# Optimization experiments

Measured on AMD Instinct MI355X. Metric: run time of the kernel, lower is better.

The kernel has to match this reference:

```python
import jax, jax.numpy as jnp
import numpy as np

B, N, F_IN, F_OUT = 4, 2048, 256, 128
ALPHA = 0.2  # LeakyReLU negative slope
EPS = 1e-5   # LayerNorm eps
NEG = -9e15


def setup_inputs() -> dict:
    key = jax.random.key(0)
    k1, k2, k3, k4 = jax.random.split(key, 4)
    h = jax.random.normal(k1, (B, N, F_IN), dtype=jnp.float32)
    adj = jax.random.randint(k2, (B, N, N), 0, 2, dtype=jnp.int32)
    # xavier_uniform with gain=1.414 for W
    limW = 1.414 * np.sqrt(6.0 / (F_IN + F_OUT))
    W = jax.random.uniform(k3, (F_IN, F_OUT), dtype=jnp.float32, minval=-limW, maxval=limW)
    # kaiming_uniform (leaky_relu, a=alpha, fan_in=2*F_OUT) for a
    gain = np.sqrt(2.0 / (1.0 + ALPHA ** 2))
    lima = gain * np.sqrt(3.0 / (2 * F_OUT))
    a = jax.random.uniform(k4, (2 * F_OUT, 1), dtype=jnp.float32, minval=-lima, maxval=lima)
    gamma = jnp.ones((F_OUT,), dtype=jnp.float32)
    beta = jnp.zeros((F_OUT,), dtype=jnp.float32)
    return {"h": h, "adj": adj, "W": W, "a": a, "gamma": gamma, "beta": beta}


def reference(h, adj, W, a, gamma, beta):
    Wh = jnp.einsum("bnf,fo->bno", h, W)            # [B,N,F_out]
    a1, a2 = a[:F_OUT, 0], a[F_OUT:, 0]              # [F_out] each
    s1 = Wh @ a1                                      # [B,N] score of node i
    s2 = Wh @ a2                                      # [B,N] score of node j
    # e[b,i,j] = LeakyReLU(s1[b,i] + s2[b,j])  -- avoids O(N^2*2F) concat tensor
    e = s1[:, :, None] + s2[:, None, :]
    e = jnp.where(e >= 0, e, ALPHA * e)
    e = jnp.where(adj > 0, e, NEG)
    attention = jax.nn.softmax(e, axis=2)             # [B,N,N]
    h_prime = jnp.einsum("bij,bjo->bio", attention, Wh)
    mu = jnp.mean(h_prime, axis=-1, keepdims=True)
    var = jnp.var(h_prime, axis=-1, keepdims=True)
    h_norm = (h_prime - mu) / jnp.sqrt(var + EPS) * gamma + beta
    return jax.nn.gelu(h_norm, approximate=False)
```

## Files before the change

kernel.cpp:

```cpp
#include <hip/hip_runtime.h>
#include <hip/hip_bf16.h>

typedef __attribute__((ext_vector_type(8))) short bf16x8;
typedef __attribute__((ext_vector_type(4))) float f32x4;

#define NB   4
#define NN   2048
#define FIN  256
#define FOUT 128
#define SPLIT 4
#define JCH  (NN / SPLIT)
#define NSTEP (JCH / 64)

__device__ __forceinline__ unsigned short f2bf(float f) {
    unsigned int u = __builtin_bit_cast(unsigned int, f);
    u += 0x7fffu + ((u >> 16) & 1u);
    return (unsigned short)(u >> 16);
}
__device__ __forceinline__ float bf2f(unsigned short s) {
    return __builtin_bit_cast(float, (unsigned int)s << 16);
}

__global__ __launch_bounds__(256) void k_wt(const float* __restrict__ W,
                                            unsigned short* __restrict__ WT) {
    int idx = blockIdx.x * 256 + threadIdx.x;
    int k = idx & 255, o = idx >> 8;
    WT[idx] = f2bf(W[k * FOUT + o]);
}

__global__ __launch_bounds__(256) void k_wh(const float* __restrict__ h,
                                            const float* __restrict__ a,
                                            const unsigned short* __restrict__ WT,
                                            unsigned short* __restrict__ WhB,
                                            float* __restrict__ s1,
                                            float* __restrict__ s2) {
    __shared__ unsigned short hs[16][264];
    __shared__ float s1w[4][16], s2w[4][16];
    int t = threadIdx.x, blk = blockIdx.x;
    int nglob0 = blk * 16;
    int b = nglob0 >> 11;

    const float4* h4 = (const float4*)h + (size_t)blk * 1024;
    #pragma unroll
    for (int i = 0; i < 4; ++i) {
        int idx = i * 256 + t;
        float4 v = h4[idx];
        int row = idx >> 6, c4 = (idx & 63) * 4;
        unsigned int lo = (unsigned int)f2bf(v.x) | ((unsigned int)f2bf(v.y) << 16);
        unsigned int hi = (unsigned int)f2bf(v.z) | ((unsigned int)f2bf(v.w) << 16);
        *(uint2*)&hs[row][c4] = make_uint2(lo, hi);
    }
    __syncthreads();

    int w = t >> 6, l = t & 63, lr = l & 15, lk = l >> 4;
    float a1v[2], a2v[2];
    #pragma unroll
    for (int j = 0; j < 2; ++j) {
        a1v[j] = a[(w * 2 + j) * 16 + lr];
        a2v[j] = a[FOUT + (w * 2 + j) * 16 + lr];
    }
    f32x4 acc[2] = {{0.f,0.f,0.f,0.f},{0.f,0.f,0.f,0.f}};

    #pragma unroll
    for (int kk = 0; kk < 8; ++kk) {
        int k0 = kk * 32;
        bf16x8 af = *(const bf16x8*)&hs[lr][k0 + lk * 8];
        #pragma unroll
        for (int j = 0; j < 2; ++j) {
            bf16x8 bfr = *(const bf16x8*)(WT + ((w * 2 + j) * 16 + lr) * 256 + k0 + lk * 8);
            acc[j] = __builtin_amdgcn_mfma_f32_16x16x32_bf16(af, bfr, acc[j], 0, 0, 0);
        }
    }

    int n0 = nglob0 & 2047;
    int sIdx = n0 >> 6;
    int hh   = (n0 >> 5) & 1;
    int bklo = (n0 & 31) >> 3;
    float v1[4] = {0.f,0.f,0.f,0.f}, v2[4] = {0.f,0.f,0.f,0.f};
    #pragma unroll
    for (int j = 0; j < 2; ++j) {
        int ot = w * 2 + j;
        float x0 = acc[j][0], x1 = acc[j][1], x2 = acc[j][2], x3 = acc[j][3];
        ushort4 pk;
        pk.x = f2bf(x0); pk.y = f2bf(x1); pk.z = f2bf(x2); pk.w = f2bf(x3);
        size_t fragBase = (((size_t)(b * 8 + ot) * 32 + sIdx) * 2 + hh) * 64;
        size_t lane = fragBase + lr + 16 * (bklo + (lk >> 1));
        *(ushort4*)(WhB + lane * 8 + (lk & 1) * 4) = pk;
        v1[0] += x0 * a1v[j]; v1[1] += x1 * a1v[j]; v1[2] += x2 * a1v[j]; v1[3] += x3 * a1v[j];
        v2[0] += x0 * a2v[j]; v2[1] += x1 * a2v[j]; v2[2] += x2 * a2v[j]; v2[3] += x3 * a2v[j];
    }
    #pragma unroll
    for (int m = 1; m < 16; m <<= 1)
        #pragma unroll
        for (int r = 0; r < 4; ++r) {
            v1[r] += __shfl_xor(v1[r], m);
            v2[r] += __shfl_xor(v2[r], m);
        }
    if (lr == 0)
        #pragma unroll
        for (int r = 0; r < 4; ++r) {
            s1w[w][lk * 4 + r] = v1[r];
            s2w[w][lk * 4 + r] = v2[r];
        }
    __syncthreads();
    if (t < 16) {
        s1[nglob0 + t] = s1w[0][t] + s1w[1][t] + s1w[2][t] + s1w[3][t];
        s2[nglob0 + t] = s2w[0][t] + s2w[1][t] + s2w[2][t] + s2w[3][t];
    }
}

__global__ __launch_bounds__(256) void k_attn(const int* __restrict__ adj,
                                              const unsigned short* __restrict__ WhB,
                                              const float* __restrict__ s1,
                                              const float* __restrict__ s2,
                                              unsigned short* __restrict__ num,
                                              float* __restrict__ Zp) {
    __shared__ union {
        unsigned short Ps[2][64][76];
        float hS[64][132];
    } S;
    __shared__ float s2S[JCH];

    int t = threadIdx.x, w = t >> 6, l = t & 63, lr = l & 15, lk = l >> 4;
    int bid = blockIdx.x;
    int bi = (bid >> 3) + (bid & 7) * 64;
    int part = bi >> 7, rem = bi & 127;
    int b = rem >> 5, i0 = (rem & 31) * 64, j0 = part * JCH;

    if (t < 128) ((float4*)s2S)[t] = ((const float4*)(s2 + b * NN + j0))[t];
    float s1r = s1[b * NN + i0 + w * 16 + lr];

    const int* aRow = adj + ((size_t)(b * NN) + i0 + w * 16 + lr) * NN + j0 + lk * 16;
    int4 av[2][4];
    #pragma unroll
    for (int s = 0; s < 2; ++s)
        #pragma unroll
        for (int q = 0; q < 4; ++q)
            av[s][q] = *(const int4*)(aRow + s * 64 + q * 4);

    const unsigned short* B0 = WhB + (((size_t)(b * 8 + w * 2) * 32 + part * NSTEP) * 2) * 512 + (size_t)l * 8;
    const unsigned short* B1 = B0 + (size_t)32 * 2 * 512;
    bf16x8 bB[2][2][2];
    #pragma unroll
    for (int s = 0; s < 2; ++s) {
        bB[s][0][0] = *(const bf16x8*)(B0 + s * 1024);
        bB[s][0][1] = *(const bf16x8*)(B0 + s * 1024 + 512);
        bB[s][1][0] = *(const bf16x8*)(B1 + s * 1024);
        bB[s][1][1] = *(const bf16x8*)(B1 + s * 1024 + 512);
    }

    f32x4 acc[4][2];
    #pragma unroll
    for (int rg = 0; rg < 4; ++rg) {
        acc[rg][0] = (f32x4){0.f,0.f,0.f,0.f};
        acc[rg][1] = (f32x4){0.f,0.f,0.f,0.f};
    }
    float zacc = 0.f;

    __syncthreads();

    #pragma unroll
    for (int s = 0; s < NSTEP; ++s) {
        const int slot = s & 1;
        int4 m0 = av[slot][0], m1 = av[slot][1], m2 = av[slot][2], m3 = av[slot][3];
        if (s < NSTEP - 2) {
            #pragma unroll
            for (int q = 0; q < 4; ++q)
                av[slot][q] = *(const int4*)(aRow + (s + 2) * 64 + q * 4);
        }

        {
            int mv[16] = {m0.x, m0.y, m0.z, m0.w, m1.x, m1.y, m1.z, m1.w,
                          m2.x, m2.y, m2.z, m2.w, m3.x, m3.y, m3.z, m3.w};
            const float* sp = &s2S[s * 64 + lk * 16];
            float4 f0 = *(const float4*)sp,       f1 = *(const float4*)(sp + 4);
            float4 f2 = *(const float4*)(sp + 8), f3 = *(const float4*)(sp + 12);
            float sv[16] = {f0.x,f0.y,f0.z,f0.w, f1.x,f1.y,f1.z,f1.w,
                            f2.x,f2.y,f2.z,f2.w, f3.x,f3.y,f3.z,f3.w};
            unsigned int pw[8];
            #pragma unroll
            for (int q = 0; q < 8; ++q) {
                float e0 = s1r + sv[2 * q];
                float e1 = s1r + sv[2 * q + 1];
                e0 = fmaxf(e0, 0.2f * e0);
                e1 = fmaxf(e1, 0.2f * e1);
                float p0 = (mv[2 * q]     > 0) ? __expf(e0) : 0.f;
                float p1 = (mv[2 * q + 1] > 0) ? __expf(e1) : 0.f;
                zacc += p0 + p1;
                pw[q] = (unsigned int)f2bf(p0) | ((unsigned int)f2bf(p1) << 16);
            }
            *(uint4*)&S.Ps[slot][w * 16 + lr][lk * 16]     = (uint4){pw[0], pw[1], pw[2], pw[3]};
            *(uint4*)&S.Ps[slot][w * 16 + lr][lk * 16 + 8] = (uint4){pw[4], pw[5], pw[6], pw[7]};
        }
        asm volatile("s_waitcnt lgkmcnt(0)" ::: "memory");
        __builtin_amdgcn_s_barrier();
        __builtin_amdgcn_sched_barrier(0);

        bf16x8 c00 = bB[slot][0][0], c01 = bB[slot][0][1];
        bf16x8 c10 = bB[slot][1][0], c11 = bB[slot][1][1];
        if (s < NSTEP - 2) {
            bB[slot][0][0] = *(const bf16x8*)(B0 + (s + 2) * 1024);
            bB[slot][0][1] = *(const bf16x8*)(B0 + (s + 2) * 1024 + 512);
            bB[slot][1][0] = *(const bf16x8*)(B1 + (s + 2) * 1024);
            bB[slot][1][1] = *(const bf16x8*)(B1 + (s + 2) * 1024 + 512);
        }

        #pragma unroll
        for (int rg = 0; rg < 4; ++rg) {
            bf16x8 a0 = *(const bf16x8*)&S.Ps[slot][rg * 16 + lr][lk * 8];
            bf16x8 a1 = *(const bf16x8*)&S.Ps[slot][rg * 16 + lr][32 + lk * 8];
            acc[rg][0] = __builtin_amdgcn_mfma_f32_16x16x32_bf16(a0, c00, acc[rg][0], 0, 0, 0);
            acc[rg][0] = __builtin_amdgcn_mfma_f32_16x16x32_bf16(a1, c01, acc[rg][0], 0, 0, 0);
            acc[rg][1] = __builtin_amdgcn_mfma_f32_16x16x32_bf16(a0, c10, acc[rg][1], 0, 0, 0);
            acc[rg][1] = __builtin_amdgcn_mfma_f32_16x16x32_bf16(a1, c11, acc[rg][1], 0, 0, 0);
        }
    }

    zacc += __shfl_xor(zacc, 16);
    zacc += __shfl_xor(zacc, 32);
    if (l < 16) Zp[(size_t)(part * NB + b) * NN + i0 + w * 16 + l] = zacc;

    __syncthreads();
    #pragma unroll
    for (int rg = 0; rg < 4; ++rg)
        #pragma unroll
        for (int ot2 = 0; ot2 < 2; ++ot2)
            #pragma unroll
            for (int r = 0; r < 4; ++r)
                S.hS[rg * 16 + lk * 4 + r][(w * 2 + ot2) * 16 + lr] = acc[rg][ot2][r];
    __syncthreads();

    unsigned short* np = num + ((size_t)(part * NB + b) * NN + i0) * FOUT;
    #pragma unroll
    for (int q = 0; q < 4; ++q) {
        int flat = q * 256 + t;
        int row = flat >> 4, c8 = (flat & 15) * 8;
        float4 v0 = *(const float4*)&S.hS[row][c8];
        float4 v1 = *(const float4*)&S.hS[row][c8 + 4];
        uint4 pk;
        pk.x = (unsigned int)f2bf(v0.x) | ((unsigned int)f2bf(v0.y) << 16);
        pk.y = (unsigned int)f2bf(v0.z) | ((unsigned int)f2bf(v0.w) << 16);
        pk.z = (unsigned int)f2bf(v1.x) | ((unsigned int)f2bf(v1.y) << 16);
        pk.w = (unsigned int)f2bf(v1.z) | ((unsigned int)f2bf(v1.w) << 16);
        *(uint4*)(np + (size_t)row * FOUT + c8) = pk;
    }
}

__global__ __launch_bounds__(256) void k_final(const unsigned short* __restrict__ num,
                                               const float* __restrict__ Zp,
                                               const float* __restrict__ gamma,
                                               const float* __restrict__ beta,
                                               float* __restrict__ out) {
    int t = threadIdx.x, bi = blockIdx.x;
    int rowA = t >> 5;
    int c0 = (t & 31) * 4;
    size_t gn = (size_t)bi * 8 + rowA;
    int b = (int)(gn >> 11), n = (int)(gn & 2047);

    float Z = 0.f;
    #pragma unroll
    for (int p = 0; p < SPLIT; ++p) Z += Zp[(size_t)(p * NB + b) * NN + n];

    float x[4] = {0.f, 0.f, 0.f, 0.f};
    #pragma unroll
    for (int p = 0; p < SPLIT; ++p) {
        const unsigned short* np = num + ((size_t)(p * NB + b) * NN + n) * FOUT + c0;
        ushort4 u = *(const ushort4*)np;
        x[0] += bf2f(u.x); x[1] += bf2f(u.y); x[2] += bf2f(u.z); x[3] += bf2f(u.w);
    }
    float rz = 1.f / Z;
    #pragma unroll
    for (int i = 0; i < 4; ++i) x[i] *= rz;

    float sm = 0.f, sq = 0.f;
    #pragma unroll
    for (int i = 0; i < 4; ++i) { sm += x[i]; sq += x[i] * x[i]; }
    #pragma unroll
    for (int m = 1; m < 32; m <<= 1) {
        sm += __shfl_xor(sm, m);
        sq += __shfl_xor(sq, m);
    }
    float mu  = sm * (1.f / 128.f);
    float var = sq * (1.f / 128.f) - mu * mu;
    float rs  = rsqrtf(var + 1e-5f);
    float4 g0 = *(const float4*)(gamma + c0);
    float4 e0 = *(const float4*)(beta + c0);
    float gg[4] = {g0.x, g0.y, g0.z, g0.w};
    float bb[4] = {e0.x, e0.y, e0.z, e0.w};
    float y[4];
    #pragma unroll
    for (int i = 0; i < 4; ++i) {
        float v = (x[i] - mu) * rs * gg[i] + bb[i];
        y[i] = 0.5f * v * (1.f + erff(v * 0.70710678118f));
    }
    float* op = out + gn * FOUT + c0;
    *(float4*)op = make_float4(y[0], y[1], y[2], y[3]);
}

extern "C" void kernel_launch(void* const* d_in, const int* in_sizes, int n_in,
                              void* d_out, int out_size, void* d_ws, size_t ws_size,
                              hipStream_t stream) {
    const float* h     = (const float*)d_in[0];
    const int*   adj   = (const int*)d_in[1];
    const float* W     = (const float*)d_in[2];
    const float* a     = (const float*)d_in[3];
    const float* gamma = (const float*)d_in[4];
    const float* beta  = (const float*)d_in[5];
    float* out = (float*)d_out;

    char* ws = (char*)d_ws;
    unsigned short* WT  = (unsigned short*)ws;
    unsigned short* WhB = (unsigned short*)(ws + (1u << 16));
    float* s1 = (float*)(ws + 2162688);
    float* s2 = (float*)(ws + 2195456);
    float* Zp = (float*)(ws + 2228224);
    unsigned short* num = (unsigned short*)(ws + 2359296);

    hipLaunchKernelGGL(k_wt,    dim3(128),  dim3(256), 0, stream, W, WT);
    hipLaunchKernelGGL(k_wh,    dim3(512),  dim3(256), 0, stream, h, a, WT, WhB, s1, s2);
    hipLaunchKernelGGL(k_attn,  dim3(512),  dim3(256), 0, stream, adj, WhB, s1, s2, num, Zp);
    hipLaunchKernelGGL(k_final, dim3(1024), dim3(256), 0, stream, num, Zp, gamma, beta, out);
}
```

Baseline: 39.56 us.

## Double attention block to 512 threads, splitting score and MFMA work per wave

The attention kernel now launches 8 waves per block instead of 4. Each wave computes probabilities for half of a 16-row by 64-column tile and handles one 16-column output slice in the MFMA stage. This halves per-thread register use and adj loads and doubles latency hiding per block. In exchange, partial row sums double to eight partitions, so the workspace layout shifts and the final kernel sums more Zp partials.

```diff
diff --git a/kernel.cpp b/kernel.cpp
--- a/kernel.cpp
+++ b/kernel.cpp
@@ -109,7 +109,7 @@
     }
 }
 
-__global__ __launch_bounds__(256) void k_attn(const int* __restrict__ adj,
+__global__ __launch_bounds__(512) void k_attn(const int* __restrict__ adj,
                                               const unsigned short* __restrict__ WhB,
                                               const float* __restrict__ s1,
                                               const float* __restrict__ s2,
@@ -127,34 +127,31 @@
     int part = bi >> 7, rem = bi & 127;
     int b = rem >> 5, i0 = (rem & 31) * 64, j0 = part * JCH;
 
+    int rg0 = w >> 1;
+    int jh  = w & 1;
+
     if (t < 128) ((float4*)s2S)[t] = ((const float4*)(s2 + b * NN + j0))[t];
-    float s1r = s1[b * NN + i0 + w * 16 + lr];
-
-    const int* aRow = adj + ((size_t)(b * NN) + i0 + w * 16 + lr) * NN + j0 + lk * 16;
-    int4 av[2][4];
-    #pragma unroll
-    for (int s = 0; s < 2; ++s)
-        #pragma unroll
-        for (int q = 0; q < 4; ++q)
-            av[s][q] = *(const int4*)(aRow + s * 64 + q * 4);
-
-    const unsigned short* B0 = WhB + (((size_t)(b * 8 + w * 2) * 32 + part * NSTEP) * 2) * 512 + (size_t)l * 8;
-    const unsigned short* B1 = B0 + (size_t)32 * 2 * 512;
-    bf16x8 bB[2][2][2];
+    float s1r = s1[b * NN + i0 + rg0 * 16 + lr];
+
+    const int* aRow = adj + ((size_t)(b * NN) + i0 + rg0 * 16 + lr) * NN + j0 + jh * 32 + lk * 8;
+    int4 av[2][2];
     #pragma unroll
     for (int s = 0; s < 2; ++s) {
-        bB[s][0][0] = *(const bf16x8*)(B0 + s * 1024);
-        bB[s][0][1] = *(const bf16x8*)(B0 + s * 1024 + 512);
-        bB[s][1][0] = *(const bf16x8*)(B1 + s * 1024);
-        bB[s][1][1] = *(const bf16x8*)(B1 + s * 1024 + 512);
-    }
-
-    f32x4 acc[4][2];
-    #pragma unroll
-    for (int rg = 0; rg < 4; ++rg) {
-        acc[rg][0] = (f32x4){0.f,0.f,0.f,0.f};
-        acc[rg][1] = (f32x4){0.f,0.f,0.f,0.f};
-    }
+        av[s][0] = *(const int4*)(aRow + s * 64);
+        av[s][1] = *(const int4*)(aRow + s * 64 + 4);
+    }
+
+    const unsigned short* Bb = WhB + (((size_t)(b * 8 + w) * 32 + part * NSTEP) * 2) * 512 + (size_t)l * 8;
+    bf16x8 bB[2][2];
+    #pragma unroll
+    for (int s = 0; s < 2; ++s) {
+        bB[s][0] = *(const bf16x8*)(Bb + s * 1024);
+        bB[s][1] = *(const bf16x8*)(Bb + s * 1024 + 512);
+    }
+
+    f32x4 acc[4];
+    #pragma unroll
+    for (int rg = 0; rg < 4; ++rg) acc[rg] = (f32x4){0.f, 0.f, 0.f, 0.f};
     float zacc = 0.f;
 
     __syncthreads();
@@ -162,24 +159,20 @@
     #pragma unroll
     for (int s = 0; s < NSTEP; ++s) {
         const int slot = s & 1;
-        int4 m0 = av[slot][0], m1 = av[slot][1], m2 = av[slot][2], m3 = av[slot][3];
+        int4 m0 = av[slot][0], m1 = av[slot][1];
         if (s < NSTEP - 2) {
+            av[slot][0] = *(const int4*)(aRow + (s + 2) * 64);
+            av[slot][1] = *(const int4*)(aRow + (s + 2) * 64 + 4);
+        }
+
+        {
+            int mv[8] = {m0.x, m0.y, m0.z, m0.w, m1.x, m1.y, m1.z, m1.w};
+            const float* sp = &s2S[s * 64 + jh * 32 + lk * 8];
+            float4 f0 = *(const float4*)sp, f1 = *(const float4*)(sp + 4);
+            float sv[8] = {f0.x, f0.y, f0.z, f0.w, f1.x, f1.y, f1.z, f1.w};
+            unsigned int pw[4];
             #pragma unroll
-            for (int q = 0; q < 4; ++q)
-                av[slot][q] = *(const int4*)(aRow + (s + 2) * 64 + q * 4);
-        }
-
-        {
-            int mv[16] = {m0.x, m0.y, m0.z, m0.w, m1.x, m1.y, m1.z, m1.w,
-                          m2.x, m2.y, m2.z, m2.w, m3.x, m3.y, m3.z, m3.w};
-            const float* sp = &s2S[s * 64 + lk * 16];
-            float4 f0 = *(const float4*)sp,       f1 = *(const float4*)(sp + 4);
-            float4 f2 = *(const float4*)(sp + 8), f3 = *(const float4*)(sp + 12);
-            float sv[16] = {f0.x,f0.y,f0.z,f0.w, f1.x,f1.y,f1.z,f1.w,
-                            f2.x,f2.y,f2.z,f2.w, f3.x,f3.y,f3.z,f3.w};
-            unsigned int pw[8];
-            #pragma unroll
-            for (int q = 0; q < 8; ++q) {
+            for (int q = 0; q < 4; ++q) {
                 float e0 = s1r + sv[2 * q];
                 float e1 = s1r + sv[2 * q + 1];
                 e0 = fmaxf(e0, 0.2f * e0);
@@ -189,51 +182,44 @@
                 zacc += p0 + p1;
                 pw[q] = (unsigned int)f2bf(p0) | ((unsigned int)f2bf(p1) << 16);
             }
-            *(uint4*)&S.Ps[slot][w * 16 + lr][lk * 16]     = (uint4){pw[0], pw[1], pw[2], pw[3]};
-            *(uint4*)&S.Ps[slot][w * 16 + lr][lk * 16 + 8] = (uint4){pw[4], pw[5], pw[6], pw[7]};
+            *(uint4*)&S.Ps[slot][rg0 * 16 + lr][jh * 32 + lk * 8] = (uint4){pw[0], pw[1], pw[2], pw[3]};
         }
         asm volatile("s_waitcnt lgkmcnt(0)" ::: "memory");
         __builtin_amdgcn_s_barrier();
         __builtin_amdgcn_sched_barrier(0);
 
-        bf16x8 c00 = bB[slot][0][0], c01 = bB[slot][0][1];
-        bf16x8 c10 = bB[slot][1][0], c11 = bB[slot][1][1];
+        bf16x8 c0 = bB[slot][0], c1 = bB[slot][1];
         if (s < NSTEP - 2) {
-            bB[slot][0][0] = *(const bf16x8*)(B0 + (s + 2) * 1024);
-            bB[slot][0][1] = *(const bf16x8*)(B0 + (s + 2) * 1024 + 512);
-            bB[slot][1][0] = *(const bf16x8*)(B1 + (s + 2) * 1024);
-            bB[slot][1][1] = *(const bf16x8*)(B1 + (s + 2) * 1024 + 512);
+            bB[slot][0] = *(const bf16x8*)(Bb + (s + 2) * 1024);
+            bB[slot][1] = *(const bf16x8*)(Bb + (s + 2) * 1024 + 512);
         }
 
         #pragma unroll
         for (int rg = 0; rg < 4; ++rg) {
             bf16x8 a0 = *(const bf16x8*)&S.Ps[slot][rg * 16 + lr][lk * 8];
             bf16x8 a1 = *(const bf16x8*)&S.Ps[slot][rg * 16 + lr][32 + lk * 8];
-            acc[rg][0] = __builtin_amdgcn_mfma_f32_16x16x32_bf16(a0, c00, acc[rg][0], 0, 0, 0);
-            acc[rg][0] = __builtin_amdgcn_mfma_f32_16x16x32_bf16(a1, c01, acc[rg][0], 0, 0, 0);
-            acc[rg][1] = __builtin_amdgcn_mfma_f32_16x16x32_bf16(a0, c10, acc[rg][1], 0, 0, 0);
-            acc[rg][1] = __builtin_amdgcn_mfma_f32_16x16x32_bf16(a1, c11, acc[rg][1], 0, 0, 0);
+            acc[rg] = __builtin_amdgcn_mfma_f32_16x16x32_bf16(a0, c0, acc[rg], 0, 0, 0);
+            acc[rg] = __builtin_amdgcn_mfma_f32_16x16x32_bf16(a1, c1, acc[rg], 0, 0, 0);
         }
     }
 
     zacc += __shfl_xor(zacc, 16);
     zacc += __shfl_xor(zacc, 32);
-    if (l < 16) Zp[(size_t)(part * NB + b) * NN + i0 + w * 16 + l] = zacc;
+    if (l < 16)
+        Zp[(size_t)((part * 2 + jh) * NB + b) * NN + i0 + rg0 * 16 + l] = zacc;
 
     __syncthreads();
     #pragma unroll
     for (int rg = 0; rg < 4; ++rg)
         #pragma unroll
-        for (int ot2 = 0; ot2 < 2; ++ot2)
-            #pragma unroll
-            for (int r = 0; r < 4; ++r)
-                S.hS[rg * 16 + lk * 4 + r][(w * 2 + ot2) * 16 + lr] = acc[rg][ot2][r];
+        for (int r = 0; r < 4; ++r)
+            S.hS[rg * 16 + lk * 4 + r][w * 16 + lr] = acc[rg][r];
     __syncthreads();
 
     unsigned short* np = num + ((size_t)(part * NB + b) * NN + i0) * FOUT;
     #pragma unroll
-    for (int q = 0; q < 4; ++q) {
-        int flat = q * 256 + t;
+    for (int q = 0; q < 2; ++q) {
+        int flat = q * 512 + t;
         int row = flat >> 4, c8 = (flat & 15) * 8;
         float4 v0 = *(const float4*)&S.hS[row][c8];
         float4 v1 = *(const float4*)&S.hS[row][c8 + 4];
@@ -259,7 +245,7 @@
 
     float Z = 0.f;
     #pragma unroll
-    for (int p = 0; p < SPLIT; ++p) Z += Zp[(size_t)(p * NB + b) * NN + n];
+    for (int p = 0; p < 2 * SPLIT; ++p) Z += Zp[(size_t)(p * NB + b) * NN + n];
 
     float x[4] = {0.f, 0.f, 0.f, 0.f};
     #pragma unroll
@@ -314,10 +300,10 @@
     float* s1 = (float*)(ws + 2162688);
     float* s2 = (float*)(ws + 2195456);
     float* Zp = (float*)(ws + 2228224);
-    unsigned short* num = (unsigned short*)(ws + 2359296);
+    unsigned short* num = (unsigned short*)(ws + 2490368);
 
     hipLaunchKernelGGL(k_wt,    dim3(128),  dim3(256), 0, stream, W, WT);
     hipLaunchKernelGGL(k_wh,    dim3(512),  dim3(256), 0, stream, h, a, WT, WhB, s1, s2);
-    hipLaunchKernelGGL(k_attn,  dim3(512),  dim3(256), 0, stream, adj, WhB, s1, s2, num, Zp);
+    hipLaunchKernelGGL(k_attn,  dim3(512),  dim3(512), 0, stream, adj, WhB, s1, s2, num, Zp);
     hipLaunchKernelGGL(k_final, dim3(1024), dim3(256), 0, stream, num, Zp, gamma, beta, out);
 }
```

Result: slower. 41.16 us (+4.1%).
